# Optimization experiments

Hardware: AMD Instinct MI355X
Metric: run time of the kernel (lower is better)

Reference implementation:

```python
import jax, jax.numpy as jnp
import numpy as np

IN_F = 256
OUT_F = 256
H = 4
DH = OUT_F // H  # 64
N = 6144


def setup_inputs() -> dict:
    key = jax.random.key(0)
    ks = jax.random.split(key, 6)
    x = jax.random.normal(ks[0], (N, IN_F), dtype=jnp.float32)
    adj = jax.random.randint(ks[1], (N, N), 0, 2, dtype=jnp.int32)
    # per-head Linear(in_features, d_head): weights [H, IN_F, DH], bias [H, DH]
    W = jax.random.normal(ks[2], (H, IN_F, DH), dtype=jnp.float32) / np.sqrt(IN_F)
    Wb = jax.random.normal(ks[3], (H, DH), dtype=jnp.float32) * 0.01
    # per-head Linear(2*d_head, 1): weights [H, 2*DH], bias [H]
    A = jax.random.normal(ks[4], (H, 2 * DH), dtype=jnp.float32) / np.sqrt(2 * DH)
    Ab = jax.random.normal(ks[5], (H,), dtype=jnp.float32) * 0.01
    return {"x": x, "adj": adj, "W": W, "Wb": Wb, "A": A, "Ab": Ab}


def reference(x, adj, W, Wb, A, Ab):
    # h[h,n,d] = per-head linear projection of node features
    h = jnp.einsum("ni,hid->hnd", x, W) + Wb[:, None, :]
    a_src, a_dst = A[:, :DH], A[:, DH:]
    # score(i,j) = a_src . h_i + a_dst . h_j + b  (decomposed concat-linear)
    s_src = jnp.einsum("hnd,hd->hn", h, a_src) + Ab[:, None]  # [H, N]
    s_dst = jnp.einsum("hnd,hd->hn", h, a_dst)                # [H, N]
    scores = s_src[:, :, None] + s_dst[:, None, :]            # [H, N, N]
    # Faithful to source: non-edges get score 0.0 (not -inf) before softmax
    scores = jnp.where(adj[None, :, :] > 0, scores, 0.0)
    probs = jax.nn.softmax(scores, axis=-1)                   # row softmax
    out = jnp.einsum("hij,hjd->hid", probs, h)                # [H, N, DH]
    # concat heads along feature dim -> [N, H*DH]
    return jnp.transpose(out, (1, 0, 2)).reshape(N, H * DH)
```

## Files before the change

kernel.cpp:

```cpp
#include <hip/hip_runtime.h>
#include <stdint.h>

#define NN 6144
#define NC 576

typedef float f32x4 __attribute__((ext_vector_type(4)));
typedef __bf16 bf16x8v __attribute__((ext_vector_type(8)));

__device__ __forceinline__ unsigned short f2bf(float f) {
  unsigned u = __float_as_uint(f);
  u += 0x7FFFu + ((u >> 16) & 1u);
  return (unsigned short)(u >> 16);
}

__device__ __forceinline__ float bf2f(unsigned short s) {
  unsigned u = (unsigned)s << 16;
  return __uint_as_float(u);
}

__device__ __forceinline__ unsigned char f2e4m3(float f) {
  unsigned u = __float_as_uint(f);
  unsigned sgn = (u >> 24) & 0x80u;
  unsigned au = u & 0x7FFFFFFFu;
  if (au >= 0x43E00000u) return (unsigned char)(sgn | 0x7E);
  if (au < 0x3C800000u) {
    int q = (int)rintf(__uint_as_float(au) * 512.0f);
    return (unsigned char)(sgn | (q >= 8 ? 0x08 : q));
  }
  unsigned r = au + 0x7FFFFu + ((au >> 20) & 1u);
  int e = (int)(r >> 23) - 127;
  unsigned m = (r >> 20) & 7u;
  return (unsigned char)(sgn | ((unsigned)(e + 7) << 3) | m);
}

__device__ __forceinline__ unsigned short pack2(float a, float b) {
  return (unsigned short)f2e4m3(a) | ((unsigned short)f2e4m3(b) << 8);
}

__device__ __forceinline__ void async_load16(const void* g, void* l) {
  __builtin_amdgcn_global_load_lds(
      (__attribute__((address_space(1))) void*)(uintptr_t)g,
      (__attribute__((address_space(3))) void*)(uint32_t)(uintptr_t)l,
      16, 0, 0);
}

__global__ __launch_bounds__(256) void p0s(
    const float* __restrict__ x, const float* __restrict__ W,
    const float* __restrict__ Aw, const float* __restrict__ Wb,
    unsigned short* __restrict__ xsw, unsigned short* __restrict__ wsw,
    float* __restrict__ Acat, float* __restrict__ T)
{
  const int bid = blockIdx.x, t = threadIdx.x;
  if (bid < 8) {
#pragma unroll
    for (int i = 0; i < 4; ++i) {
      const int e = bid * 256 + t + i * 2048;
      const int l = e & 63, kc = (e >> 6) & 7, ct = e >> 9;
      const int c = ct * 16 + (l & 15);
      const int h = c >> 6, d0 = c & 63;
      const int ks = kc * 32 + (l >> 4) * 8;
      const float* src = W + h * 16384 + ks * 64 + d0;
      unsigned uu[4];
#pragma unroll
      for (int j = 0; j < 4; ++j)
        uu[j] = (unsigned)f2bf(src[(2*j) * 64]) | ((unsigned)f2bf(src[(2*j+1) * 64]) << 16);
      *(uint4*)(wsw + (size_t)e * 8) = (uint4){uu[0], uu[1], uu[2], uu[3]};
    }
    return;
  }
  if (bid == 8) {
    T[t] = 0.f;
    const int h = t >> 6, d = t & 63;
    Acat[t]       = Aw[h * 128 + d];
    Acat[256 + t] = Aw[h * 128 + 64 + d];
    Acat[512 + t] = Wb[t];
    return;
  }
  const int tid = (bid - 9) * 256 + t;
#pragma unroll
  for (int i = 0; i < 4; ++i) {
    const int e = tid + i * 49152;
    const int l = e & 63, kc = (e >> 6) & 7, mt = e >> 9;
    const int node = mt * 16 + (l & 15);
    const int ks = kc * 32 + (l >> 4) * 8;
    const float4* xp = (const float4*)(x + (size_t)node * 256 + ks);
    float4 v0 = xp[0], v1 = xp[1];
    uint4 o;
    o.x = (unsigned)f2bf(v0.x) | ((unsigned)f2bf(v0.y) << 16);
    o.y = (unsigned)f2bf(v0.z) | ((unsigned)f2bf(v0.w) << 16);
    o.z = (unsigned)f2bf(v1.x) | ((unsigned)f2bf(v1.y) << 16);
    o.w = (unsigned)f2bf(v1.z) | ((unsigned)f2bf(v1.w) << 16);
    *(uint4*)(xsw + (size_t)e * 8) = o;
  }
}

__global__ __launch_bounds__(256) void k1m(
    const unsigned short* __restrict__ xsw, const unsigned short* __restrict__ wsw,
    const float* __restrict__ Acat, const float* __restrict__ Ab,
    const int* __restrict__ adj, unsigned* __restrict__ bm,
    unsigned char* __restrict__ V8, float* __restrict__ e_src, float* __restrict__ T)
{
  __shared__ unsigned char lv[4][4096];
  __shared__ float lt[256];
  const int t = threadIdx.x;

  if (blockIdx.x >= 192) {
    const int pb = blockIdx.x - 192;
    const int tid = pb * 256 + t;
    const int4* src = (const int4*)adj + (size_t)tid * 8;
    int4 q[8];
#pragma unroll
    for (int j = 0; j < 8; ++j) q[j] = src[j];
    unsigned b = 0;
#pragma unroll
    for (int j = 0; j < 8; ++j) {
      unsigned nib = (unsigned)q[j].x | ((unsigned)q[j].y << 1) |
                     ((unsigned)q[j].z << 2) | ((unsigned)q[j].w << 3);
      b |= nib << (4 * j);
    }
    bm[tid] = b;
    return;
  }

  const int w = t >> 6, l = t & 63;
  const int v = blockIdx.x * 4 + w;
  const int mt = v >> 1, nh = v & 1;
  const int i0 = mt * 16, c0 = nh * 128;
  const int lm = l & 15, lk = l >> 4;

  lt[t] = 0.f;
  __syncthreads();

  f32x4 acc[8];
#pragma unroll
  for (int nt = 0; nt < 8; ++nt) acc[nt] = (f32x4){0.f, 0.f, 0.f, 0.f};

  const unsigned short* ap = xsw + ((size_t)mt * 512 + l) * 8;
  const unsigned short* bp = wsw + ((size_t)nh * 4096 + l) * 8;

#pragma unroll
  for (int kc = 0; kc < 8; ++kc) {
    bf16x8v a = *(const bf16x8v*)(ap + (size_t)kc * 512);
#pragma unroll
    for (int nt = 0; nt < 8; ++nt) {
      bf16x8v b = *(const bf16x8v*)(bp + ((size_t)nt * 512 + kc * 64) * 8);
      acc[nt] = __builtin_amdgcn_mfma_f32_16x16x32_bf16(a, b, acc[nt], 0, 0, 0);
    }
  }

  float asv[8], adv[8];
#pragma unroll
  for (int nt = 0; nt < 8; ++nt) {
    const int cc = c0 + nt * 16 + lm;
    const float wb = Acat[512 + cc];
#pragma unroll
    for (int rr = 0; rr < 4; ++rr) acc[nt][rr] += wb;
    asv[nt] = Acat[cc];
    adv[nt] = Acat[256 + cc];
  }

#pragma unroll
  for (int nt = 0; nt < 8; ++nt)
    atomicAdd(&lt[c0 + nt * 16 + lm], acc[nt][0] + acc[nt][1] + acc[nt][2] + acc[nt][3]);

  float ss[2][4], sd[2][4];
#pragma unroll
  for (int hl = 0; hl < 2; ++hl)
#pragma unroll
    for (int rr = 0; rr < 4; ++rr) {
      float s1 = 0.f, s2 = 0.f;
#pragma unroll
      for (int j = 0; j < 4; ++j) {
        s1 += acc[hl * 4 + j][rr] * asv[hl * 4 + j];
        s2 += acc[hl * 4 + j][rr] * adv[hl * 4 + j];
      }
      ss[hl][rr] = s1; sd[hl][rr] = s2;
    }
#pragma unroll
  for (int off = 1; off < 16; off <<= 1)
#pragma unroll
    for (int hl = 0; hl < 2; ++hl)
#pragma unroll
      for (int rr = 0; rr < 4; ++rr) {
        ss[hl][rr] += __shfl_xor(ss[hl][rr], off);
        sd[hl][rr] += __shfl_xor(sd[hl][rr], off);
      }

  float ed[2][4];
#pragma unroll
  for (int hl = 0; hl < 2; ++hl)
#pragma unroll
    for (int rr = 0; rr < 4; ++rr) ed[hl][rr] = expf(sd[hl][rr]);

  if (lm == 0) {
#pragma unroll
    for (int hl = 0; hl < 2; ++hl) {
      const int hh = nh * 2 + hl;
      const float ab = Ab[hh];
#pragma unroll
      for (int rr = 0; rr < 4; ++rr)
        e_src[(size_t)hh * NN + i0 + lk * 4 + rr] = expf(ss[hl][rr] + ab);
    }
  }

  unsigned char* mylv = lv[w];
#pragma unroll
  for (int nt = 0; nt < 8; ++nt) {
    const int hl = nt >> 2;
    const int d = (nt & 3) * 16 + lm;
    const int lcE = hl * 128 + d;
    const int lcP = lcE + 64;
    *(unsigned short*)(mylv + lcE * 16 + lk * 4)     = pack2(ed[hl][0] * acc[nt][0], ed[hl][1] * acc[nt][1]);
    *(unsigned short*)(mylv + lcE * 16 + lk * 4 + 2) = pack2(ed[hl][2] * acc[nt][2], ed[hl][3] * acc[nt][3]);
    *(unsigned short*)(mylv + lcP * 16 + lk * 4)     = pack2(acc[nt][0], acc[nt][1]);
    *(unsigned short*)(mylv + lcP * 16 + lk * 4 + 2) = pack2(acc[nt][2], acc[nt][3]);
  }
#pragma unroll
  for (int j = 0; j < 4; ++j) {
    const int lc = j * 64 + l;
    uint4 val = *(const uint4*)(mylv + lc * 16);
    *(uint4*)(V8 + (size_t)(nh * 256 + lc) * NN + i0) = val;
  }
  if (lm == 0) {
#pragma unroll
    for (int hl = 0; hl < 2; ++hl) {
      const int hh = nh * 2 + hl;
      unsigned char* pq = V8 + (size_t)(512 + hh) * NN + i0 + lk * 4;
      *(unsigned short*)pq       = pack2(ed[hl][0], ed[hl][1]);
      *(unsigned short*)(pq + 2) = pack2(ed[hl][2], ed[hl][3]);
    }
    if (nh == 0)
      *(unsigned*)(V8 + (size_t)516 * NN + i0 + lk * 4) = 0x38383838u;
  }

  __syncthreads();
  atomicAdd(&T[t], lt[t]);
}

__global__ __launch_bounds__(256, 3) void k2_gemm(
    const unsigned* __restrict__ bm, const unsigned char* __restrict__ V8,
    unsigned short* __restrict__ out2b, float* __restrict__ out2e, int nks)
{
  __shared__ unsigned char lB[144 * 128];
  const int t   = threadIdx.x;
  const int cb  = blockIdx.x & 3;
  const int rb  = (blockIdx.x >> 2) & 31;
  const int ks  = blockIdx.x >> 7;
  const int krange = NN / nks;
  const int i0 = rb * 192, n0 = cb * 144, k0 = ks * krange;
  const int w = t >> 6, l = t & 63;
  const int lm = l & 15, lk = l >> 4;

  f32x4 acc[3][9];
#pragma unroll
  for (int mt = 0; mt < 3; ++mt)
#pragma unroll
    for (int nt = 0; nt < 9; ++nt) acc[mt][nt] = (f32x4){0.f, 0.f, 0.f, 0.f};

  int scol[5], sgr[5];
#pragma unroll
  for (int u = 0; u < 5; ++u) {
    const int gi = u * 256 + t;
    scol[u] = gi >> 3;
    sgr[u]  = (gi & 7) ^ (scol[u] & 7);
  }
  const int dbase4 = (1024 + (t & ~63)) * 16;

  const unsigned* gA0 = bm + (size_t)(i0 + w * 48 + lm) * (NN / 32) + (k0 >> 5) + lk;
  const unsigned char* gBb = V8 + (size_t)n0 * NN + k0;

  const int iters = krange / 128;
  for (int it = 0; it < iters; ++it) {
    const unsigned char* gB = gBb + it * 128;
#pragma unroll
    for (int u = 0; u < 4; ++u)
      async_load16(gB + (size_t)scol[u] * NN + sgr[u] * 16,
                   (char*)lB + (size_t)(u * 256 + (t & ~63)) * 16);
    if (t < 128)
      async_load16(gB + (size_t)scol[4] * NN + sgr[4] * 16, (char*)lB + dbase4);

    unsigned bits[3];
#pragma unroll
    for (int mt = 0; mt < 3; ++mt)
      bits[mt] = gA0[(size_t)mt * 16 * (NN / 32) + it * 4];

    longlong2 afr[3][2];
#pragma unroll
    for (int mt = 0; mt < 3; ++mt) {
      unsigned u[8];
#pragma unroll
      for (int i = 0; i < 8; ++i) {
        unsigned nib = (bits[mt] >> (4 * i)) & 0xFu;
        u[i] = ((nib * 0x00204081u) & 0x01010101u) << 3;
      }
      afr[mt][0].x = (long long)(((unsigned long long)u[1] << 32) | u[0]);
      afr[mt][0].y = (long long)(((unsigned long long)u[3] << 32) | u[2]);
      afr[mt][1].x = (long long)(((unsigned long long)u[5] << 32) | u[4]);
      afr[mt][1].y = (long long)(((unsigned long long)u[7] << 32) | u[6]);
    }
    __syncthreads();
#pragma unroll
    for (int b = 0; b < 2; ++b) {
#pragma unroll
      for (int nt = 0; nt < 9; ++nt) {
        const int cc = nt * 16 + lm;
        const int pos = (lk * 2 + b) ^ (cc & 7);
        longlong2 bv = *(const longlong2*)(lB + cc * 128 + pos * 16);
#pragma unroll
        for (int mt = 0; mt < 3; ++mt) {
          acc[mt][nt] = __builtin_amdgcn_mfma_f32_16x16x32_fp8_fp8(
              afr[mt][b].x, bv.x, acc[mt][nt], 0, 0, 0);
          acc[mt][nt] = __builtin_amdgcn_mfma_f32_16x16x32_fp8_fp8(
              afr[mt][b].y, bv.y, acc[mt][nt], 0, 0, 0);
        }
      }
    }
    __syncthreads();
  }

  unsigned short* lw = (unsigned short*)(lB + w * 4608);
  float* oe = out2e + (size_t)ks * ((size_t)NN * 64);
  unsigned short* pb = out2b + ((size_t)(ks * 4 + cb) * NN + i0 + w * 48) * 144;
#pragma unroll
  for (int mt = 0; mt < 3; ++mt) {
#pragma unroll
    for (int nt = 0; nt < 9; ++nt) {
      const int coll = nt * 16 + lm;
#pragma unroll
      for (int rr = 0; rr < 4; ++rr)
        lw[(lk * 4 + rr) * 144 + coll] = f2bf(acc[mt][nt][rr] * 64.0f);
      if (cb == 3 && nt >= 5) {
        const int row = i0 + w * 48 + mt * 16 + lk * 4;
#pragma unroll
        for (int rr = 0; rr < 4; ++rr)
          oe[(size_t)(row + rr) * 64 + (n0 + coll - 512)] = acc[mt][nt][rr] * 64.0f;
      }
    }
    const uint4* ls = (const uint4*)(lB + w * 4608);
    char* dst = (char*)(pb + (size_t)mt * 16 * 144);
    for (int s = l; s < 288; s += 64)
      *(uint4*)(dst + s * 16) = ls[s];
  }
}

__global__ __launch_bounds__(256) void k3_final(
    const unsigned short* __restrict__ out2b, const float* __restrict__ out2e,
    const float* __restrict__ e_src, const float* __restrict__ T,
    float* __restrict__ out, int nks)
{
  const int n = blockIdx.x, c = threadIdx.x;
  const int h = c >> 6, d = c & 63;
  const int cS = h * 128 + d, cP = cS + 64;
  const int cbS = cS / 144, ofS = cS % 144;
  const int cbP = cP / 144, ofP = cP % 144;
  float Se = 0.f, Sp = 0.f, E = 0.f, dg = 0.f;
  for (int s = 0; s < nks; ++s) {
    const unsigned short* base = out2b + (size_t)s * 4 * NN * 144;
    Se += bf2f(base[((size_t)cbS * NN + n) * 144 + ofS]);
    Sp += bf2f(base[((size_t)cbP * NN + n) * 144 + ofP]);
    const float* re = out2e + (size_t)s * NN * 64 + (size_t)n * 64;
    E  += re[h];
    dg += re[4];
  }
  float e = e_src[h * NN + n];
  float D = e * E + ((float)NN - dg);
  out[(size_t)n * 256 + c] = (e * Se + (T[c] - Sp)) / D;
}

extern "C" void kernel_launch(void* const* d_in, const int* in_sizes, int n_in,
                              void* d_out, int out_size, void* d_ws, size_t ws_size,
                              hipStream_t stream) {
  const float* x  = (const float*)d_in[0];
  const int*   adj= (const int*)d_in[1];
  const float* W  = (const float*)d_in[2];
  const float* Wb = (const float*)d_in[3];
  const float* Aw = (const float*)d_in[4];
  const float* Ab = (const float*)d_in[5];
  float* out = (float*)d_out;
  char* ws = (char*)d_ws;
  unsigned char* V8 = (unsigned char*)ws;
  float* e_src = (float*)(ws + 3538944);
  float* T     = (float*)(ws + 3637248);
  float* Acat  = (float*)(ws + 3638272);
  unsigned short* wsw = (unsigned short*)(ws + 3641344);
  unsigned short* xsw = (unsigned short*)(ws + 3772416);
  unsigned* bm = (unsigned*)(ws + 6918144);
  unsigned short* out2b = (unsigned short*)(ws + 44666880);
  float* out2e = (float*)(ws + 87134208);

  const size_t slabB = (size_t)4 * NN * 144 * 2;
  const size_t slabE = (size_t)NN * 64 * 4;
  int nks = 2;
  if (ws_size >= 87134208 + 6 * slabE)                    nks = 6;
  else if (ws_size >= 44666880 + 4 * slabB + 4 * slabE)   nks = 4;

  hipLaunchKernelGGL(p0s, dim3(201), dim3(256), 0, stream,
                     x, W, Aw, Wb, xsw, wsw, Acat, T);
  hipLaunchKernelGGL(k1m, dim3(4800), dim3(256), 0, stream,
                     xsw, wsw, Acat, Ab, adj, bm, V8, e_src, T);
  hipLaunchKernelGGL(k2_gemm, dim3(128 * nks), dim3(256), 0, stream, bm, V8, out2b, out2e, nks);
  hipLaunchKernelGGL(k3_final, dim3(NN), dim3(256), 0, stream, out2b, out2e, e_src, T, out, nks);
}
```

Measured before the change: 277.9 us.

## Double-buffer LDS tiles in k2_gemm to overlap next-stage loads with MFMA

Doubles the shared-memory B tile and prefetches the next k-step's fp8 values and adjacency bitmask words while the current tile feeds the MFMAs. This removes the barrier between issuing loads and computing, so global/async load latency can hide behind the MFMA work. Each iteration now needs one barrier instead of two. The cost is double the LDS per block (about 36KB), which could reduce occupancy against the 3-blocks-per-CU launch bound, plus a few extra registers for the prefetched bitmask words.

```diff
diff --git a/kernel.cpp b/kernel.cpp
--- a/kernel.cpp
+++ b/kernel.cpp
@@ -241,7 +241,7 @@
     const unsigned* __restrict__ bm, const unsigned char* __restrict__ V8,
     unsigned short* __restrict__ out2b, float* __restrict__ out2e, int nks)
 {
-  __shared__ unsigned char lB[144 * 128];
+  __shared__ unsigned char lB[2][144 * 128];
   const int t   = threadIdx.x;
   const int cb  = blockIdx.x & 3;
   const int rb  = (blockIdx.x >> 2) & 31;
@@ -270,19 +270,33 @@
   const unsigned char* gBb = V8 + (size_t)n0 * NN + k0;
 
   const int iters = krange / 128;
+
+#define K2_STAGE(BUF, IT)                                                        \
+  do {                                                                           \
+    const unsigned char* gB = gBb + (IT) * 128;                                  \
+    _Pragma("unroll")                                                            \
+    for (int u = 0; u < 4; ++u)                                                  \
+      async_load16(gB + (size_t)scol[u] * NN + sgr[u] * 16,                      \
+                   (char*)lB[BUF] + (size_t)(u * 256 + (t & ~63)) * 16);         \
+    if (t < 128)                                                                 \
+      async_load16(gB + (size_t)scol[4] * NN + sgr[4] * 16,                      \
+                   (char*)lB[BUF] + dbase4);                                     \
+  } while (0)
+
+  unsigned bits_c[3], bits_n[3];
+  K2_STAGE(0, 0);
+#pragma unroll
+  for (int mt = 0; mt < 3; ++mt) bits_c[mt] = gA0[(size_t)mt * 16 * (NN / 32)];
+  __syncthreads();
+
+  int cur = 0;
   for (int it = 0; it < iters; ++it) {
-    const unsigned char* gB = gBb + it * 128;
-#pragma unroll
-    for (int u = 0; u < 4; ++u)
-      async_load16(gB + (size_t)scol[u] * NN + sgr[u] * 16,
-                   (char*)lB + (size_t)(u * 256 + (t & ~63)) * 16);
-    if (t < 128)
-      async_load16(gB + (size_t)scol[4] * NN + sgr[4] * 16, (char*)lB + dbase4);
-
-    unsigned bits[3];
-#pragma unroll
-    for (int mt = 0; mt < 3; ++mt)
-      bits[mt] = gA0[(size_t)mt * 16 * (NN / 32) + it * 4];
+    if (it + 1 < iters) {
+      K2_STAGE(cur ^ 1, it + 1);
+#pragma unroll
+      for (int mt = 0; mt < 3; ++mt)
+        bits_n[mt] = gA0[(size_t)mt * 16 * (NN / 32) + (it + 1) * 4];
+    }
 
     longlong2 afr[3][2];
 #pragma unroll
@@ -290,7 +304,7 @@
       unsigned u[8];
 #pragma unroll
       for (int i = 0; i < 8; ++i) {
-        unsigned nib = (bits[mt] >> (4 * i)) & 0xFu;
+        unsigned nib = (bits_c[mt] >> (4 * i)) & 0xFu;
         u[i] = ((nib * 0x00204081u) & 0x01010101u) << 3;
       }
       afr[mt][0].x = (long long)(((unsigned long long)u[1] << 32) | u[0]);
@@ -298,14 +312,14 @@
       afr[mt][1].x = (long long)(((unsigned long long)u[5] << 32) | u[4]);
       afr[mt][1].y = (long long)(((unsigned long long)u[7] << 32) | u[6]);
     }
-    __syncthreads();
+
 #pragma unroll
     for (int b = 0; b < 2; ++b) {
 #pragma unroll
       for (int nt = 0; nt < 9; ++nt) {
         const int cc = nt * 16 + lm;
         const int pos = (lk * 2 + b) ^ (cc & 7);
-        longlong2 bv = *(const longlong2*)(lB + cc * 128 + pos * 16);
+        longlong2 bv = *(const longlong2*)(lB[cur] + cc * 128 + pos * 16);
 #pragma unroll
         for (int mt = 0; mt < 3; ++mt) {
           acc[mt][nt] = __builtin_amdgcn_mfma_f32_16x16x32_fp8_fp8(
@@ -315,10 +329,17 @@
         }
       }
     }
+
+    if (it + 1 < iters) {
+#pragma unroll
+      for (int mt = 0; mt < 3; ++mt) bits_c[mt] = bits_n[mt];
+    }
     __syncthreads();
-  }
-
-  unsigned short* lw = (unsigned short*)(lB + w * 4608);
+    cur ^= 1;
+  }
+#undef K2_STAGE
+
+  unsigned short* lw = (unsigned short*)((char*)lB[0] + w * 4608);
   float* oe = out2e + (size_t)ks * ((size_t)NN * 64);
   unsigned short* pb = out2b + ((size_t)(ks * 4 + cb) * NN + i0 + w * 48) * 144;
 #pragma unroll
@@ -336,7 +357,7 @@
           oe[(size_t)(row + rr) * 64 + (n0 + coll - 512)] = acc[mt][nt][rr] * 64.0f;
       }
     }
-    const uint4* ls = (const uint4*)(lB + w * 4608);
+    const uint4* ls = (const uint4*)((char*)lB[0] + w * 4608);
     char* dst = (char*)(pb + (size_t)mt * 16 * 144);
     for (int s = l; s < 288; s += 64)
       *(uint4*)(dst + s * 16) = ls[s];
```

New measurement: 275.5 us. No clear change (-0.9%).
